# Kernel tuning notes

Hardware: AMD Instinct MI355X
Metric: run time of the kernel (lower is better)

Reference implementation:

```python
import jax, jax.numpy as jnp
import numpy as np

N, M, K, D, H, C = 100000, 10000, 32, 64, 8, 64


def setup_inputs() -> dict:
    key = jax.random.key(0)
    ks = jax.random.split(key, 7)
    x = jax.random.normal(ks[0], (N, D), dtype=jnp.float32)
    src_idx = jax.random.randint(ks[1], (M, K), 0, N)
    dst_idx = jax.random.randint(ks[2], (M,), 0, N)
    # Linear weights stored as [in, out] (y = x @ W), matching torch Linear math
    Wq = jax.random.normal(ks[3], (D, D), dtype=jnp.float32) / np.sqrt(D)
    Wk = jax.random.normal(ks[4], (D, D * H), dtype=jnp.float32) / np.sqrt(D)
    Wp1 = jax.random.normal(ks[5], (H, H), dtype=jnp.float32) / np.sqrt(H)
    Wp2 = jax.random.normal(ks[6], (H, C), dtype=jnp.float32) / np.sqrt(H)
    return {"x": x, "src_idx": src_idx, "dst_idx": dst_idx,
            "Wq": Wq, "Wk": Wk, "Wp1": Wp1, "Wp2": Wp2}


def reference(x, src_idx, dst_idx, Wq, Wk, Wp1, Wp2):
    # gather destination / source node features (irregular access)
    n_i = x[dst_idx] @ Wq                              # [M, D]
    n_j = (x[src_idx] @ Wk).reshape(M, K, H, D)        # [M, K, H, D]
    # multi-head QK pair score, scaled by sqrt(dim)
    pair = jnp.einsum('md,mkhd->mkh', n_i, n_j) / jnp.sqrt(jnp.asarray(D, x.dtype))
    # small MLP head (dropout in eval mode = identity)
    hidden = jax.nn.relu(pair @ Wp1)                   # [M, K, H]
    logits = (hidden @ Wp2).reshape(M * K, C)          # [M*K, C]
    return logits
```

## Files before the change

### kernel.cpp

```cpp
#include <hip/hip_runtime.h>


#define Mm 10000
#define Kk 32
#define Dd 64
#define Hh 8
#define Cc 64

constexpr int M_PER_A2 = 20;
constexpr size_t WC_FLOATS = 64 * 512;
constexpr size_t A_FLOATS  = (size_t)Mm * 512;
constexpr size_t WS_NEED   = (WC_FLOATS + A_FLOATS) * sizeof(float);

__global__ __launch_bounds__(256) void wc_build(
    const float* __restrict__ Wq,
    const float* __restrict__ Wk,
    float* __restrict__ WC)
{
    __shared__ float wq_l[16][68];
    __shared__ float wk_l[64][68];

    const int t  = threadIdx.x;
    const int e0 = blockIdx.x * 16;
    const int h  = blockIdx.y;

    {
        int r = t >> 4, q = t & 15;
        float4 v = ((const float4*)Wq)[(e0 + r) * 16 + q];
        *(float4*)&wq_l[r][q * 4] = v;
    }
    #pragma unroll
    for (int p = 0; p < 4; ++p) {
        int task = p * 256 + t;
        int dp = task >> 4, q = task & 15;
        float4 v = ((const float4*)Wk)[(size_t)dp * 128 + h * 16 + q];
        *(float4*)&wk_l[dp][q * 4] = v;
    }
    __syncthreads();

    const int dp = t & 63;
    const int eq = t >> 6;

    float4 wr[16];
    #pragma unroll
    for (int d4 = 0; d4 < 16; ++d4) wr[d4] = *(const float4*)&wk_l[dp][d4 * 4];

    #pragma unroll
    for (int i = 0; i < 4; ++i) {
        const int er = eq * 4 + i;
        float acc = 0.f;
        #pragma unroll
        for (int d4 = 0; d4 < 16; ++d4) {
            float4 qv = *(const float4*)&wq_l[er][d4 * 4];
            acc = fmaf(qv.x, wr[d4].x, acc);
            acc = fmaf(qv.y, wr[d4].y, acc);
            acc = fmaf(qv.z, wr[d4].z, acc);
            acc = fmaf(qv.w, wr[d4].w, acc);
        }
        WC[(size_t)(e0 + er) * 512 + h * 64 + dp] = acc * 0.125f;
    }
}

__global__ __launch_bounds__(512) void disto_A2(
    const float* __restrict__ x,
    const int*   __restrict__ dst_idx,
    const float* __restrict__ WC,
    float* __restrict__ A)
{
    __shared__ float xr[M_PER_A2][68];

    const int t  = threadIdx.x;
    const int m0 = blockIdx.x * M_PER_A2;

    if (t < M_PER_A2 * 16) {
        int r = t >> 4, q = t & 15;
        int idx = dst_idx[m0 + r];
        float4 v = ((const float4*)x)[(size_t)idx * 16 + q];
        *(float4*)&xr[r][q * 4] = v;
    }

    float wc[64];
    #pragma unroll
    for (int e = 0; e < 64; ++e) wc[e] = WC[(size_t)e * 512 + t];

    __syncthreads();

    for (int mi = 0; mi < M_PER_A2; ++mi) {
        float acc0 = 0.f, acc1 = 0.f;
        #pragma unroll
        for (int e4 = 0; e4 < 16; ++e4) {
            float4 xv = *(const float4*)&xr[mi][e4 * 4];
            acc0 = fmaf(xv.x, wc[e4 * 4 + 0], acc0);
            acc1 = fmaf(xv.y, wc[e4 * 4 + 1], acc1);
            acc0 = fmaf(xv.z, wc[e4 * 4 + 2], acc0);
            acc1 = fmaf(xv.w, wc[e4 * 4 + 3], acc1);
        }
        A[(size_t)(m0 + mi) * 512 + t] = acc0 + acc1;
    }
}

__global__ __launch_bounds__(256) void disto_B(
    const float* __restrict__ x,
    const int*   __restrict__ src_idx,
    const float* __restrict__ A,
    const float* __restrict__ Wp1,
    const float* __restrict__ Wp2,
    float* __restrict__ out)
{
    __shared__ float a_lds[Hh][68];
    __shared__ float xs[Kk][68];
    __shared__ float wp2[Hh * Cc];

    const int t = threadIdx.x;
    const int m = blockIdx.x;
    const int w = t >> 6;
    const int l = t & 63;

    if (t < 128) {
        float4 v = ((const float4*)A)[(size_t)m * 128 + t];
        *(float4*)&a_lds[t >> 4][(t & 15) * 4] = v;
    } else {
        ((float4*)wp2)[t - 128] = ((const float4*)Wp2)[t - 128];
    }
    #pragma unroll
    for (int p = 0; p < 2; ++p) {
        int task = p * 256 + t;
        int r = task >> 4, q = task & 15;
        int idx = src_idx[m * Kk + r];
        float4 v = ((const float4*)x)[(size_t)idx * 16 + q];
        *(float4*)&xs[r][q * 4] = v;
    }

    const int h_role = l & 7;
    const int k8     = l >> 3;
    float wp1r[8];
    #pragma unroll
    for (int jj = 0; jj < 8; ++jj) wp1r[jj] = Wp1[h_role * Hh + jj];

    __syncthreads();

    const int k = w * 8 + k8;
    float pair = 0.f;
    {
        const float4* xr4 = (const float4*)xs[k];
        const float4* ar  = (const float4*)a_lds[h_role];
        #pragma unroll
        for (int d4 = 0; d4 < 16; ++d4) {
            float4 xv = xr4[d4];
            float4 av = ar[d4];
            pair = fmaf(xv.x, av.x, pair);
            pair = fmaf(xv.y, av.y, pair);
            pair = fmaf(xv.z, av.z, pair);
            pair = fmaf(xv.w, av.w, pair);
        }
    }

    float hid[8];
    #pragma unroll
    for (int jj = 0; jj < 8; ++jj) hid[jj] = pair * wp1r[jj];
    #pragma unroll
    for (int s = 1; s < 8; s <<= 1) {
        #pragma unroll
        for (int jj = 0; jj < 8; ++jj)
            hid[jj] += __shfl_xor(hid[jj], s, 64);
    }
    #pragma unroll
    for (int jj = 0; jj < 8; ++jj) hid[jj] = fmaxf(hid[jj], 0.f);

    float lg[8] = {0,0,0,0,0,0,0,0};
    #pragma unroll
    for (int hp = 0; hp < 8; ++hp) {
        const float* wrow = &wp2[hp * Cc + h_role * 8];
        float4 wa = *(const float4*)wrow;
        float4 wb = *(const float4*)(wrow + 4);
        lg[0] = fmaf(hid[hp], wa.x, lg[0]);
        lg[1] = fmaf(hid[hp], wa.y, lg[1]);
        lg[2] = fmaf(hid[hp], wa.z, lg[2]);
        lg[3] = fmaf(hid[hp], wa.w, lg[3]);
        lg[4] = fmaf(hid[hp], wb.x, lg[4]);
        lg[5] = fmaf(hid[hp], wb.y, lg[5]);
        lg[6] = fmaf(hid[hp], wb.z, lg[6]);
        lg[7] = fmaf(hid[hp], wb.w, lg[7]);
    }
    size_t row = (size_t)m * Kk + k;
    float4* o4 = (float4*)(out + row * Cc + h_role * 8);
    o4[0] = make_float4(lg[0], lg[1], lg[2], lg[3]);
    o4[1] = make_float4(lg[4], lg[5], lg[6], lg[7]);
}

constexpr int WAVES = 4;
constexpr int PAD = 68;

__global__ __launch_bounds__(256) void disto_fused(
    const float* __restrict__ x,
    const int*   __restrict__ src_idx,
    const int*   __restrict__ dst_idx,
    const float* __restrict__ Wq,
    const float* __restrict__ Wk,
    const float* __restrict__ Wp1,
    const float* __restrict__ Wp2,
    float* __restrict__ out)
{
    __shared__ float ni_lds[WAVES][Dd];
    __shared__ float A_lds[WAVES][Hh][PAD];
    __shared__ float xs_lds[WAVES][8][PAD];
    __shared__ float wp2_lds[Hh * Cc];

    const int t = threadIdx.x;
    const int w = t >> 6;
    const int l = t & 63;
    const int m = blockIdx.x * WAVES + w;

    if (t < 128) ((float4*)wp2_lds)[t] = ((const float4*)Wp2)[t];

    const int dst = dst_idx[m];
    float xd = x[(size_t)dst * Dd + l];
    float acc1 = 0.f;
    #pragma unroll
    for (int dp = 0; dp < Dd; ++dp) {
        float xv = __shfl(xd, dp, 64);
        acc1 = fmaf(xv, Wq[dp * Dd + l], acc1);
    }
    ni_lds[w][l] = acc1;
    __syncthreads();
    {
        const float4* ni4 = (const float4*)ni_lds[w];
        const float4* wkrow = (const float4*)(Wk + (size_t)l * (Dd * Hh));
        #pragma unroll
        for (int h = 0; h < Hh; ++h) {
            float a = 0.f;
            #pragma unroll
            for (int d4 = 0; d4 < Dd / 4; ++d4) {
                float4 nv = ni4[d4];
                float4 wv = wkrow[h * (Dd / 4) + d4];
                a = fmaf(nv.x, wv.x, a);
                a = fmaf(nv.y, wv.y, a);
                a = fmaf(nv.z, wv.z, a);
                a = fmaf(nv.w, wv.w, a);
            }
            A_lds[w][h][l] = a * 0.125f;
        }
    }
    const int h_role = l & 7;
    const int k8 = l >> 3;
    float wp1r[8];
    #pragma unroll
    for (int j = 0; j < 8; ++j) wp1r[j] = Wp1[h_role * Hh + j];
    __syncthreads();

    for (int kc = 0; kc < 4; ++kc) {
        #pragma unroll
        for (int p = 0; p < 2; ++p) {
            int task = p * 64 + l;
            int r = task >> 4;
            int j = task & 15;
            int idx = src_idx[m * Kk + kc * 8 + r];
            float4 v = ((const float4*)x)[(size_t)idx * (Dd / 4) + j];
            *(float4*)&xs_lds[w][r][j * 4] = v;
        }
        __syncthreads();
        float pair = 0.f;
        {
            const float4* xsr = (const float4*)xs_lds[w][k8];
            const float4* ar  = (const float4*)A_lds[w][h_role];
            #pragma unroll
            for (int d4 = 0; d4 < Dd / 4; ++d4) {
                float4 xv = xsr[d4];
                float4 av = ar[d4];
                pair = fmaf(xv.x, av.x, pair);
                pair = fmaf(xv.y, av.y, pair);
                pair = fmaf(xv.z, av.z, pair);
                pair = fmaf(xv.w, av.w, pair);
            }
        }
        float hid[8];
        #pragma unroll
        for (int j = 0; j < 8; ++j) hid[j] = pair * wp1r[j];
        #pragma unroll
        for (int s = 1; s < 8; s <<= 1) {
            #pragma unroll
            for (int j = 0; j < 8; ++j)
                hid[j] += __shfl_xor(hid[j], s, 64);
        }
        #pragma unroll
        for (int j = 0; j < 8; ++j) hid[j] = fmaxf(hid[j], 0.f);
        float lg[8] = {0,0,0,0,0,0,0,0};
        #pragma unroll
        for (int hp = 0; hp < 8; ++hp) {
            const float* wrow = &wp2_lds[hp * Cc + h_role * 8];
            float4 wa = *(const float4*)wrow;
            float4 wb = *(const float4*)(wrow + 4);
            lg[0] = fmaf(hid[hp], wa.x, lg[0]);
            lg[1] = fmaf(hid[hp], wa.y, lg[1]);
            lg[2] = fmaf(hid[hp], wa.z, lg[2]);
            lg[3] = fmaf(hid[hp], wa.w, lg[3]);
            lg[4] = fmaf(hid[hp], wb.x, lg[4]);
            lg[5] = fmaf(hid[hp], wb.y, lg[5]);
            lg[6] = fmaf(hid[hp], wb.z, lg[6]);
            lg[7] = fmaf(hid[hp], wb.w, lg[7]);
        }
        size_t row = (size_t)(m * Kk + kc * 8 + k8);
        float4* o4 = (float4*)(out + row * Cc + h_role * 8);
        o4[0] = make_float4(lg[0], lg[1], lg[2], lg[3]);
        o4[1] = make_float4(lg[4], lg[5], lg[6], lg[7]);
        __syncthreads();
    }
}

extern "C" void kernel_launch(void* const* d_in, const int* in_sizes, int n_in,
                              void* d_out, int out_size, void* d_ws, size_t ws_size,
                              hipStream_t stream) {
    const float* x       = (const float*)d_in[0];
    const int*   src_idx = (const int*)  d_in[1];
    const int*   dst_idx = (const int*)  d_in[2];
    const float* Wq      = (const float*)d_in[3];
    const float* Wk      = (const float*)d_in[4];
    const float* Wp1     = (const float*)d_in[5];
    const float* Wp2     = (const float*)d_in[6];
    float* out = (float*)d_out;

    if (ws_size >= WS_NEED) {
        float* WC = (float*)d_ws;
        float* A  = WC + WC_FLOATS;
        wc_build<<<dim3(4, 8), dim3(256), 0, stream>>>(Wq, Wk, WC);
        disto_A2<<<dim3(Mm / M_PER_A2), dim3(512), 0, stream>>>(x, dst_idx, WC, A);
        disto_B<<<dim3(Mm), dim3(256), 0, stream>>>(x, src_idx, A, Wp1, Wp2, out);
    } else {
        disto_fused<<<dim3(Mm / WAVES), dim3(256), 0, stream>>>(
            x, src_idx, dst_idx, Wq, Wk, Wp1, Wp2, out);
    }
}
```

Measured before the change: 156.8 us.

## Restructure disto_B to one row per wave with register-resident A and no LDS

disto_B now gives each wave one m row instead of giving each block one row. Lanes split the D dimension in 8-wide slices, keep their slice of A (all 8 heads) and all of Wp1 in registers, and combine per-head partial dot products with xor shuffles. Gathered x rows are loaded straight into registers and double-buffered so the next load overlaps the current compute, which removes LDS staging and the block barrier. The trade-offs are heavier register use and more shuffles per k, and M_PER_A2 is also halved to give the A2 kernel more blocks.

```diff
diff --git a/kernel.cpp b/kernel.cpp
--- a/kernel.cpp
+++ b/kernel.cpp
@@ -7,7 +7,7 @@
 #define Hh 8
 #define Cc 64
 
-constexpr int M_PER_A2 = 20;
+constexpr int M_PER_A2 = 10;
 constexpr size_t WC_FLOATS = 64 * 512;
 constexpr size_t A_FLOATS  = (size_t)Mm * 512;
 constexpr size_t WS_NEED   = (WC_FLOATS + A_FLOATS) * sizeof(float);
@@ -107,85 +107,97 @@
     const float* __restrict__ Wp2,
     float* __restrict__ out)
 {
-    __shared__ float a_lds[Hh][68];
-    __shared__ float xs[Kk][68];
-    __shared__ float wp2[Hh * Cc];
-
-    const int t = threadIdx.x;
-    const int m = blockIdx.x;
-    const int w = t >> 6;
-    const int l = t & 63;
-
-    if (t < 128) {
-        float4 v = ((const float4*)A)[(size_t)m * 128 + t];
-        *(float4*)&a_lds[t >> 4][(t & 15) * 4] = v;
-    } else {
-        ((float4*)wp2)[t - 128] = ((const float4*)Wp2)[t - 128];
-    }
-    #pragma unroll
-    for (int p = 0; p < 2; ++p) {
-        int task = p * 256 + t;
-        int r = task >> 4, q = task & 15;
-        int idx = src_idx[m * Kk + r];
-        float4 v = ((const float4*)x)[(size_t)idx * 16 + q];
-        *(float4*)&xs[r][q * 4] = v;
-    }
-
-    const int h_role = l & 7;
-    const int k8     = l >> 3;
-    float wp1r[8];
-    #pragma unroll
-    for (int jj = 0; jj < 8; ++jj) wp1r[jj] = Wp1[h_role * Hh + jj];
-
-    __syncthreads();
-
-    const int k = w * 8 + k8;
-    float pair = 0.f;
-    {
-        const float4* xr4 = (const float4*)xs[k];
-        const float4* ar  = (const float4*)a_lds[h_role];
-        #pragma unroll
-        for (int d4 = 0; d4 < 16; ++d4) {
-            float4 xv = xr4[d4];
-            float4 av = ar[d4];
-            pair = fmaf(xv.x, av.x, pair);
-            pair = fmaf(xv.y, av.y, pair);
-            pair = fmaf(xv.z, av.z, pair);
-            pair = fmaf(xv.w, av.w, pair);
-        }
-    }
-
-    float hid[8];
-    #pragma unroll
-    for (int jj = 0; jj < 8; ++jj) hid[jj] = pair * wp1r[jj];
-    #pragma unroll
-    for (int s = 1; s < 8; s <<= 1) {
-        #pragma unroll
-        for (int jj = 0; jj < 8; ++jj)
-            hid[jj] += __shfl_xor(hid[jj], s, 64);
-    }
-    #pragma unroll
-    for (int jj = 0; jj < 8; ++jj) hid[jj] = fmaxf(hid[jj], 0.f);
-
-    float lg[8] = {0,0,0,0,0,0,0,0};
-    #pragma unroll
-    for (int hp = 0; hp < 8; ++hp) {
-        const float* wrow = &wp2[hp * Cc + h_role * 8];
-        float4 wa = *(const float4*)wrow;
-        float4 wb = *(const float4*)(wrow + 4);
-        lg[0] = fmaf(hid[hp], wa.x, lg[0]);
-        lg[1] = fmaf(hid[hp], wa.y, lg[1]);
-        lg[2] = fmaf(hid[hp], wa.z, lg[2]);
-        lg[3] = fmaf(hid[hp], wa.w, lg[3]);
-        lg[4] = fmaf(hid[hp], wb.x, lg[4]);
-        lg[5] = fmaf(hid[hp], wb.y, lg[5]);
-        lg[6] = fmaf(hid[hp], wb.z, lg[6]);
-        lg[7] = fmaf(hid[hp], wb.w, lg[7]);
-    }
-    size_t row = (size_t)m * Kk + k;
-    float4* o4 = (float4*)(out + row * Cc + h_role * 8);
-    o4[0] = make_float4(lg[0], lg[1], lg[2], lg[3]);
-    o4[1] = make_float4(lg[4], lg[5], lg[6], lg[7]);
+    const int t  = threadIdx.x;
+    const int w  = t >> 6;
+    const int l  = t & 63;
+    const int m  = blockIdx.x * 4 + w;
+    const int j  = l & 7;
+    const int k8 = l >> 3;
+
+    int idx[4];
+    #pragma unroll
+    for (int kc = 0; kc < 4; ++kc) idx[kc] = src_idx[m * Kk + kc * 8 + k8];
+
+    float a[8][8];
+    #pragma unroll
+    for (int h = 0; h < 8; ++h) {
+        float4 u = ((const float4*)A)[(size_t)m * 128 + h * 16 + j * 2];
+        float4 v = ((const float4*)A)[(size_t)m * 128 + h * 16 + j * 2 + 1];
+        a[h][0] = u.x; a[h][1] = u.y; a[h][2] = u.z; a[h][3] = u.w;
+        a[h][4] = v.x; a[h][5] = v.y; a[h][6] = v.z; a[h][7] = v.w;
+    }
+
+    float wp1[8][8];
+    #pragma unroll
+    for (int h = 0; h < 8; ++h) {
+        float4 u = *(const float4*)(Wp1 + h * 8);
+        float4 v = *(const float4*)(Wp1 + h * 8 + 4);
+        wp1[h][0] = u.x; wp1[h][1] = u.y; wp1[h][2] = u.z; wp1[h][3] = u.w;
+        wp1[h][4] = v.x; wp1[h][5] = v.y; wp1[h][6] = v.z; wp1[h][7] = v.w;
+    }
+
+    float xr0[8], xr1[8];
+    auto load_x = [&](float* xr, int id) {
+        const float4* p = (const float4*)(x + (size_t)id * 64 + j * 8);
+        float4 u = p[0], v = p[1];
+        xr[0] = u.x; xr[1] = u.y; xr[2] = u.z; xr[3] = u.w;
+        xr[4] = v.x; xr[5] = v.y; xr[6] = v.z; xr[7] = v.w;
+    };
+    auto compute = [&](const float* xr, int kc) {
+        float partial[8];
+        #pragma unroll
+        for (int h = 0; h < 8; ++h) {
+            float p0 = 0.f, p1 = 0.f;
+            #pragma unroll
+            for (int i = 0; i < 8; i += 2) {
+                p0 = fmaf(xr[i],     a[h][i],     p0);
+                p1 = fmaf(xr[i + 1], a[h][i + 1], p1);
+            }
+            partial[h] = p0 + p1;
+        }
+        #pragma unroll
+        for (int s = 1; s < 8; s <<= 1) {
+            #pragma unroll
+            for (int h = 0; h < 8; ++h)
+                partial[h] += __shfl_xor(partial[h], s, 64);
+        }
+        float hid[8];
+        #pragma unroll
+        for (int jp = 0; jp < 8; ++jp) {
+            float s0 = 0.f;
+            #pragma unroll
+            for (int h = 0; h < 8; ++h)
+                s0 = fmaf(partial[h], wp1[h][jp], s0);
+            hid[jp] = fmaxf(s0, 0.f);
+        }
+        float lg[8] = {0,0,0,0,0,0,0,0};
+        #pragma unroll
+        for (int h = 0; h < 8; ++h) {
+            float4 wa = ((const float4*)Wp2)[h * 16 + j * 2];
+            float4 wb = ((const float4*)Wp2)[h * 16 + j * 2 + 1];
+            lg[0] = fmaf(hid[h], wa.x, lg[0]);
+            lg[1] = fmaf(hid[h], wa.y, lg[1]);
+            lg[2] = fmaf(hid[h], wa.z, lg[2]);
+            lg[3] = fmaf(hid[h], wa.w, lg[3]);
+            lg[4] = fmaf(hid[h], wb.x, lg[4]);
+            lg[5] = fmaf(hid[h], wb.y, lg[5]);
+            lg[6] = fmaf(hid[h], wb.z, lg[6]);
+            lg[7] = fmaf(hid[h], wb.w, lg[7]);
+        }
+        size_t row = (size_t)m * Kk + kc * 8 + k8;
+        float4* o4 = (float4*)(out + row * Cc + j * 8);
+        o4[0] = make_float4(lg[0], lg[1], lg[2], lg[3]);
+        o4[1] = make_float4(lg[4], lg[5], lg[6], lg[7]);
+    };
+
+    load_x(xr0, idx[0]);
+    load_x(xr1, idx[1]);
+    compute(xr0, 0);
+    load_x(xr0, idx[2]);
+    compute(xr1, 1);
+    load_x(xr1, idx[3]);
+    compute(xr0, 2);
+    compute(xr1, 3);
 }
 
 constexpr int WAVES = 4;
@@ -245,7 +257,7 @@
     const int k8 = l >> 3;
     float wp1r[8];
     #pragma unroll
-    for (int j = 0; j < 8; ++j) wp1r[j] = Wp1[h_role * Hh + j];
+    for (int jj = 0; jj < 8; ++jj) wp1r[jj] = Wp1[h_role * Hh + jj];
     __syncthreads();
 
     for (int kc = 0; kc < 4; ++kc) {
@@ -253,10 +265,10 @@
         for (int p = 0; p < 2; ++p) {
             int task = p * 64 + l;
             int r = task >> 4;
-            int j = task & 15;
+            int jq = task & 15;
             int idx = src_idx[m * Kk + kc * 8 + r];
-            float4 v = ((const float4*)x)[(size_t)idx * (Dd / 4) + j];
-            *(float4*)&xs_lds[w][r][j * 4] = v;
+            float4 v = ((const float4*)x)[(size_t)idx * (Dd / 4) + jq];
+            *(float4*)&xs_lds[w][r][jq * 4] = v;
         }
         __syncthreads();
         float pair = 0.f;
@@ -275,15 +287,15 @@
         }
         float hid[8];
         #pragma unroll
-        for (int j = 0; j < 8; ++j) hid[j] = pair * wp1r[j];
+        for (int jj = 0; jj < 8; ++jj) hid[jj] = pair * wp1r[jj];
         #pragma unroll
         for (int s = 1; s < 8; s <<= 1) {
             #pragma unroll
-            for (int j = 0; j < 8; ++j)
-                hid[j] += __shfl_xor(hid[j], s, 64);
-        }
-        #pragma unroll
-        for (int j = 0; j < 8; ++j) hid[j] = fmaxf(hid[j], 0.f);
+            for (int jj = 0; jj < 8; ++jj)
+                hid[jj] += __shfl_xor(hid[jj], s, 64);
+        }
+        #pragma unroll
+        for (int jj = 0; jj < 8; ++jj) hid[jj] = fmaxf(hid[jj], 0.f);
         float lg[8] = {0,0,0,0,0,0,0,0};
         #pragma unroll
         for (int hp = 0; hp < 8; ++hp) {
@@ -324,7 +336,7 @@
         float* A  = WC + WC_FLOATS;
         wc_build<<<dim3(4, 8), dim3(256), 0, stream>>>(Wq, Wk, WC);
         disto_A2<<<dim3(Mm / M_PER_A2), dim3(512), 0, stream>>>(x, dst_idx, WC, A);
-        disto_B<<<dim3(Mm), dim3(256), 0, stream>>>(x, src_idx, A, Wp1, Wp2, out);
+        disto_B<<<dim3(Mm / 4), dim3(256), 0, stream>>>(x, src_idx, A, Wp1, Wp2, out);
     } else {
         disto_fused<<<dim3(Mm / WAVES), dim3(256), 0, stream>>>(
             x, src_idx, dst_idx, Wq, Wk, Wp1, Wp2, out);
```

Result: slower. 177.1 us (+13.0%).

## Fuse A projection and pair-score kernels with double-buffered gather prefetch

Applied to the files above, without the earlier changes.

Merges the per-destination projection kernel and the per-edge score/MLP kernel into one 512-thread kernel that handles 16 destinations per block. The intermediate A tensor is no longer written to and read back from global memory. Source and destination rows for the next pair of destinations are prefetched into registers and stored to a double-buffered LDS area while the current pair is computed. The cost is fewer blocks (625), a 64-float register array for WC in every thread, and larger LDS use, which may reduce occupancy.

```diff
diff --git a/kernel.cpp b/kernel.cpp
--- a/kernel.cpp
+++ b/kernel.cpp
@@ -7,10 +7,10 @@
 #define Hh 8
 #define Cc 64
 
-constexpr int M_PER_A2 = 20;
+constexpr int MB_ = 16;
+constexpr int PAIRS = 8;
 constexpr size_t WC_FLOATS = 64 * 512;
-constexpr size_t A_FLOATS  = (size_t)Mm * 512;
-constexpr size_t WS_NEED   = (WC_FLOATS + A_FLOATS) * sizeof(float);
+constexpr size_t WS_NEED = WC_FLOATS * sizeof(float);
 
 __global__ __launch_bounds__(256) void wc_build(
     const float* __restrict__ Wq,
@@ -61,131 +61,144 @@
     }
 }
 
-__global__ __launch_bounds__(512) void disto_A2(
+__global__ __launch_bounds__(512) void disto_AB(
     const float* __restrict__ x,
+    const int*   __restrict__ src_idx,
     const int*   __restrict__ dst_idx,
     const float* __restrict__ WC,
-    float* __restrict__ A)
-{
-    __shared__ float xr[M_PER_A2][68];
-
-    const int t  = threadIdx.x;
-    const int m0 = blockIdx.x * M_PER_A2;
-
-    if (t < M_PER_A2 * 16) {
-        int r = t >> 4, q = t & 15;
-        int idx = dst_idx[m0 + r];
-        float4 v = ((const float4*)x)[(size_t)idx * 16 + q];
-        *(float4*)&xr[r][q * 4] = v;
-    }
-
-    float wc[64];
-    #pragma unroll
-    for (int e = 0; e < 64; ++e) wc[e] = WC[(size_t)e * 512 + t];
-
-    __syncthreads();
-
-    for (int mi = 0; mi < M_PER_A2; ++mi) {
-        float acc0 = 0.f, acc1 = 0.f;
-        #pragma unroll
-        for (int e4 = 0; e4 < 16; ++e4) {
-            float4 xv = *(const float4*)&xr[mi][e4 * 4];
-            acc0 = fmaf(xv.x, wc[e4 * 4 + 0], acc0);
-            acc1 = fmaf(xv.y, wc[e4 * 4 + 1], acc1);
-            acc0 = fmaf(xv.z, wc[e4 * 4 + 2], acc0);
-            acc1 = fmaf(xv.w, wc[e4 * 4 + 3], acc1);
-        }
-        A[(size_t)(m0 + mi) * 512 + t] = acc0 + acc1;
-    }
-}
-
-__global__ __launch_bounds__(256) void disto_B(
-    const float* __restrict__ x,
-    const int*   __restrict__ src_idx,
-    const float* __restrict__ A,
     const float* __restrict__ Wp1,
     const float* __restrict__ Wp2,
     float* __restrict__ out)
 {
-    __shared__ float a_lds[Hh][68];
-    __shared__ float xs[Kk][68];
-    __shared__ float wp2[Hh * Cc];
-
-    const int t = threadIdx.x;
-    const int m = blockIdx.x;
-    const int w = t >> 6;
-    const int l = t & 63;
-
-    if (t < 128) {
-        float4 v = ((const float4*)A)[(size_t)m * 128 + t];
-        *(float4*)&a_lds[t >> 4][(t & 15) * 4] = v;
-    } else {
-        ((float4*)wp2)[t - 128] = ((const float4*)Wp2)[t - 128];
-    }
+    __shared__ float xs[2][64][68];
+    __shared__ float dstx[2][2][68];
+    __shared__ float a_lds[2][8][68];
+    __shared__ float wp2_l[512];
+    __shared__ int   idx_l[MB_ * Kk];
+    __shared__ int   didx_l[MB_];
+
+    const int t  = threadIdx.x;
+    const int m0 = blockIdx.x * MB_;
+
+    idx_l[t] = src_idx[m0 * Kk + t];
+    if (t < MB_) didx_l[t] = dst_idx[m0 + t];
+    if (t < 128) ((float4*)wp2_l)[t] = ((const float4*)Wp2)[t];
+
+    float wc[64];
+    #pragma unroll
+    for (int e = 0; e < 64; ++e) wc[e] = WC[(size_t)e * 512 + t];
+
+    __syncthreads();
+
     #pragma unroll
     for (int p = 0; p < 2; ++p) {
-        int task = p * 256 + t;
+        int task = p * 512 + t;
         int r = task >> 4, q = task & 15;
-        int idx = src_idx[m * Kk + r];
-        float4 v = ((const float4*)x)[(size_t)idx * 16 + q];
-        *(float4*)&xs[r][q * 4] = v;
-    }
-
-    const int h_role = l & 7;
-    const int k8     = l >> 3;
+        float4 v = ((const float4*)x)[(size_t)idx_l[r] * 16 + q];
+        *(float4*)&xs[0][r][q * 4] = v;
+    }
+    if (t < 32) {
+        float4 v = ((const float4*)x)[(size_t)didx_l[t >> 4] * 16 + (t & 15)];
+        *(float4*)&dstx[0][t >> 4][(t & 15) * 4] = v;
+    }
+
+    const int l = t & 63, w = t >> 6;
+    const int ml_w = w >> 2, ch = w & 3;
+    const int h_role = l & 7, k8 = l >> 3;
     float wp1r[8];
     #pragma unroll
-    for (int jj = 0; jj < 8; ++jj) wp1r[jj] = Wp1[h_role * Hh + jj];
-
-    __syncthreads();
-
-    const int k = w * 8 + k8;
-    float pair = 0.f;
-    {
-        const float4* xr4 = (const float4*)xs[k];
-        const float4* ar  = (const float4*)a_lds[h_role];
-        #pragma unroll
-        for (int d4 = 0; d4 < 16; ++d4) {
-            float4 xv = xr4[d4];
-            float4 av = ar[d4];
-            pair = fmaf(xv.x, av.x, pair);
-            pair = fmaf(xv.y, av.y, pair);
-            pair = fmaf(xv.z, av.z, pair);
-            pair = fmaf(xv.w, av.w, pair);
-        }
-    }
-
-    float hid[8];
-    #pragma unroll
-    for (int jj = 0; jj < 8; ++jj) hid[jj] = pair * wp1r[jj];
-    #pragma unroll
-    for (int s = 1; s < 8; s <<= 1) {
-        #pragma unroll
-        for (int jj = 0; jj < 8; ++jj)
-            hid[jj] += __shfl_xor(hid[jj], s, 64);
-    }
-    #pragma unroll
-    for (int jj = 0; jj < 8; ++jj) hid[jj] = fmaxf(hid[jj], 0.f);
-
-    float lg[8] = {0,0,0,0,0,0,0,0};
-    #pragma unroll
-    for (int hp = 0; hp < 8; ++hp) {
-        const float* wrow = &wp2[hp * Cc + h_role * 8];
-        float4 wa = *(const float4*)wrow;
-        float4 wb = *(const float4*)(wrow + 4);
-        lg[0] = fmaf(hid[hp], wa.x, lg[0]);
-        lg[1] = fmaf(hid[hp], wa.y, lg[1]);
-        lg[2] = fmaf(hid[hp], wa.z, lg[2]);
-        lg[3] = fmaf(hid[hp], wa.w, lg[3]);
-        lg[4] = fmaf(hid[hp], wb.x, lg[4]);
-        lg[5] = fmaf(hid[hp], wb.y, lg[5]);
-        lg[6] = fmaf(hid[hp], wb.z, lg[6]);
-        lg[7] = fmaf(hid[hp], wb.w, lg[7]);
-    }
-    size_t row = (size_t)m * Kk + k;
-    float4* o4 = (float4*)(out + row * Cc + h_role * 8);
-    o4[0] = make_float4(lg[0], lg[1], lg[2], lg[3]);
-    o4[1] = make_float4(lg[4], lg[5], lg[6], lg[7]);
+    for (int j = 0; j < 8; ++j) wp1r[j] = Wp1[h_role * Hh + j];
+
+    __syncthreads();
+
+    const int hh = t >> 6, dp = t & 63;
+    int cur = 0;
+
+    for (int p = 0; p < PAIRS; ++p) {
+        float4 nx0, nx1, nd;
+        const bool havepf = (p + 1 < PAIRS);
+        const int r0 = t >> 4, q0 = t & 15;
+        const int r1 = 32 + (t >> 4);
+        if (havepf) {
+            const int base = (p + 1) * 64;
+            nx0 = ((const float4*)x)[(size_t)idx_l[base + r0] * 16 + q0];
+            nx1 = ((const float4*)x)[(size_t)idx_l[base + r1] * 16 + q0];
+            if (t < 32)
+                nd = ((const float4*)x)[(size_t)didx_l[(p + 1) * 2 + (t >> 4)] * 16 + (t & 15)];
+        }
+
+        #pragma unroll
+        for (int ml = 0; ml < 2; ++ml) {
+            float a0 = 0.f, a1 = 0.f;
+            #pragma unroll
+            for (int e4 = 0; e4 < 16; ++e4) {
+                float4 xv = *(const float4*)&dstx[cur][ml][e4 * 4];
+                a0 = fmaf(xv.x, wc[e4 * 4 + 0], a0);
+                a1 = fmaf(xv.y, wc[e4 * 4 + 1], a1);
+                a0 = fmaf(xv.z, wc[e4 * 4 + 2], a0);
+                a1 = fmaf(xv.w, wc[e4 * 4 + 3], a1);
+            }
+            a_lds[ml][hh][dp] = a0 + a1;
+        }
+        __syncthreads();
+
+        {
+            float pair = 0.f;
+            const float4* xr = (const float4*)xs[cur][ml_w * 32 + ch * 8 + k8];
+            const float4* ar = (const float4*)a_lds[ml_w][h_role];
+            #pragma unroll
+            for (int d4 = 0; d4 < 16; ++d4) {
+                float4 xv = xr[d4];
+                float4 av = ar[d4];
+                pair = fmaf(xv.x, av.x, pair);
+                pair = fmaf(xv.y, av.y, pair);
+                pair = fmaf(xv.z, av.z, pair);
+                pair = fmaf(xv.w, av.w, pair);
+            }
+            float hid[8];
+            #pragma unroll
+            for (int j = 0; j < 8; ++j) hid[j] = pair * wp1r[j];
+            #pragma unroll
+            for (int s = 1; s < 8; s <<= 1) {
+                #pragma unroll
+                for (int j = 0; j < 8; ++j)
+                    hid[j] += __shfl_xor(hid[j], s, 64);
+            }
+            #pragma unroll
+            for (int j = 0; j < 8; ++j) hid[j] = fmaxf(hid[j], 0.f);
+
+            float lg[8] = {0, 0, 0, 0, 0, 0, 0, 0};
+            #pragma unroll
+            for (int hp = 0; hp < 8; ++hp) {
+                const float* wrow = &wp2_l[hp * Cc + h_role * 8];
+                float4 wa = *(const float4*)wrow;
+                float4 wb = *(const float4*)(wrow + 4);
+                lg[0] = fmaf(hid[hp], wa.x, lg[0]);
+                lg[1] = fmaf(hid[hp], wa.y, lg[1]);
+                lg[2] = fmaf(hid[hp], wa.z, lg[2]);
+                lg[3] = fmaf(hid[hp], wa.w, lg[3]);
+                lg[4] = fmaf(hid[hp], wb.x, lg[4]);
+                lg[5] = fmaf(hid[hp], wb.y, lg[5]);
+                lg[6] = fmaf(hid[hp], wb.z, lg[6]);
+                lg[7] = fmaf(hid[hp], wb.w, lg[7]);
+            }
+            const int m = m0 + p * 2 + ml_w;
+            size_t row = (size_t)m * Kk + ch * 8 + k8;
+            float4* o4 = (float4*)(out + row * Cc + h_role * 8);
+            o4[0] = make_float4(lg[0], lg[1], lg[2], lg[3]);
+            o4[1] = make_float4(lg[4], lg[5], lg[6], lg[7]);
+        }
+
+        if (havepf) {
+            const int nxt = cur ^ 1;
+            *(float4*)&xs[nxt][r0][q0 * 4] = nx0;
+            *(float4*)&xs[nxt][r1][q0 * 4] = nx1;
+            if (t < 32)
+                *(float4*)&dstx[nxt][t >> 4][(t & 15) * 4] = nd;
+        }
+        __syncthreads();
+        cur ^= 1;
+    }
 }
 
 constexpr int WAVES = 4;
@@ -253,10 +266,10 @@
         for (int p = 0; p < 2; ++p) {
             int task = p * 64 + l;
             int r = task >> 4;
-            int j = task & 15;
+            int jq = task & 15;
             int idx = src_idx[m * Kk + kc * 8 + r];
-            float4 v = ((const float4*)x)[(size_t)idx * (Dd / 4) + j];
-            *(float4*)&xs_lds[w][r][j * 4] = v;
+            float4 v = ((const float4*)x)[(size_t)idx * (Dd / 4) + jq];
+            *(float4*)&xs_lds[w][r][jq * 4] = v;
         }
         __syncthreads();
         float pair = 0.f;
@@ -321,10 +334,9 @@
 
     if (ws_size >= WS_NEED) {
         float* WC = (float*)d_ws;
-        float* A  = WC + WC_FLOATS;
         wc_build<<<dim3(4, 8), dim3(256), 0, stream>>>(Wq, Wk, WC);
-        disto_A2<<<dim3(Mm / M_PER_A2), dim3(512), 0, stream>>>(x, dst_idx, WC, A);
-        disto_B<<<dim3(Mm), dim3(256), 0, stream>>>(x, src_idx, A, Wp1, Wp2, out);
+        disto_AB<<<dim3(Mm / MB_), dim3(512), 0, stream>>>(
+            x, src_idx, dst_idx, WC, Wp1, Wp2, out);
     } else {
         disto_fused<<<dim3(Mm / WAVES), dim3(256), 0, stream>>>(
             x, src_idx, dst_idx, Wq, Wk, Wp1, Wp2, out);
```

After: 160.4 us. 2.3% more time.
